# Kernel optimization log

Measured on AMD Instinct MI355X. Metric: run time of the kernel, lower is better.

## Reference

```python
import jax, jax.numpy as jnp
import numpy as np

N, S, D = 100000, 4, 256
TAU, ITERS = 0.1, 10
EPS = 1e-12  # torch F.normalize default eps


def sinkhorn_knopp(H_raw, tau=TAU, num_iters=ITERS):
    # H_raw: (N, S, S) -> doubly stochastic via exp + alternating row/col normalization
    M = jnp.exp(H_raw / tau)
    def body(_, M):
        M = M / jnp.sum(M, axis=-1, keepdims=True)  # row normalize
        M = M / jnp.sum(M, axis=-2, keepdims=True)  # col normalize
        return M
    return jax.lax.fori_loop(0, num_iters, body, M)


def setup_inputs() -> dict:
    key = jax.random.key(0)
    ks = jax.random.split(key, 7)
    x_streams = jax.random.normal(ks[0], (N, S, D), jnp.float32)
    message_output = jax.random.normal(ks[1], (N, D), jnp.float32)
    theta_pre = jax.random.normal(ks[2], (1, D), jnp.float32) * 0.01
    b_pre = jnp.ones((1, S), jnp.float32) / S
    theta_post = jax.random.normal(ks[3], (1, D), jnp.float32) * 0.01
    b_post = jnp.ones((1, S), jnp.float32) / S
    Theta_res = jax.random.normal(ks[4], (S, D), jnp.float32) * 0.01
    B_res = jnp.eye(S, dtype=jnp.float32) + jax.random.normal(ks[5], (S, S), jnp.float32) * 0.01
    alpha = jnp.asarray(0.01, jnp.float32)
    return {
        'x_streams': x_streams, 'message_output': message_output,
        'theta_pre': theta_pre, 'b_pre': b_pre,
        'theta_post': theta_post, 'b_post': b_post,
        'Theta_res': Theta_res, 'B_res': B_res,
        'alpha_pre': alpha, 'alpha_post': alpha, 'alpha_res': alpha,
    }


def reference(x_streams, message_output, theta_pre, b_pre, theta_post, b_post,
              Theta_res, B_res, alpha_pre, alpha_post, alpha_res):
    x = x_streams  # (N, S, D)
    # F.normalize(x, p=2, dim=-1)
    x_norm = x / jnp.maximum(jnp.linalg.norm(x, axis=-1, keepdims=True), EPS)
    x_pooled = x_norm.mean(axis=1)  # (N, D)

    # H_pre / H_post: (N, 1, S)
    dyn_pre = jnp.tanh(x_pooled @ theta_pre.T)   # (N, 1)
    H_pre = alpha_pre * dyn_pre[..., None] + b_pre[None, :, :]
    dyn_post = jnp.tanh(x_pooled @ theta_post.T)  # (N, 1)
    H_post = alpha_post * dyn_post[..., None] + b_post[None, :, :]

    # H_res: (N, S, S), doubly stochastic
    dyn_res = jnp.tanh(x_pooled @ Theta_res.T)   # (N, S)
    H_res_raw = alpha_res * dyn_res[..., None] + B_res[None, :, :]
    H_res = sinkhorn_knopp(H_res_raw, TAU, ITERS)

    residual = jnp.einsum('nst,ntd->nsd', H_res, x)          # bmm
    message_expanded = jnp.swapaxes(H_post, 1, 2) * message_output[:, None, :]  # (N,S,1)*(N,1,D)
    x_streams_new = residual + message_expanded
    return (x_streams_new, H_pre)
```

## Files before the change

### kernel.cpp

```cpp
#include <hip/hip_runtime.h>
#include <math.h>

static constexpr int DD = 256;

__device__ __forceinline__ float tanh_fast(float x) {
    float e = __expf(2.0f * x);
    return 1.0f - 2.0f * __builtin_amdgcn_rcpf(e + 1.0f);
}
__device__ __forceinline__ float dot4(float4 a, float4 b) {
    return a.x * b.x + a.y * b.y + a.z * b.z + a.w * b.w;
}
__device__ __forceinline__ float rl(float v, int l) {
    return __int_as_float(__builtin_amdgcn_readlane(__float_as_int(v), l));
}

__global__ __launch_bounds__(256) void hyperconn_kernel(
    const float* __restrict__ x_streams,
    const float* __restrict__ message_output,
    const float* __restrict__ theta_pre,
    const float* __restrict__ b_pre,
    const float* __restrict__ theta_post,
    const float* __restrict__ b_post,
    const float* __restrict__ Theta_res,
    const float* __restrict__ B_res,
    const float* __restrict__ alpha_pre_p,
    const float* __restrict__ alpha_post_p,
    const float* __restrict__ alpha_res_p,
    float* __restrict__ out_x,
    float* __restrict__ out_hpre,
    int Ntot)
{
    const int lane = threadIdx.x & 63;
    const int w = threadIdx.x >> 6;
    const long long n = (long long)blockIdx.x * 4 + w;
    const bool valid = (n < (long long)Ntot);

    __shared__ float sdots[4][8];
    __shared__ __align__(16) float sM[4][16];
    __shared__ __align__(16) float sHpost[4][4];

    float4 x0, x1, x2, x3, mv;
    if (valid) {
        const float4* xp = reinterpret_cast<const float4*>(x_streams + n * (4 * DD));
        x0 = xp[0 * 64 + lane];
        x1 = xp[1 * 64 + lane];
        x2 = xp[2 * 64 + lane];
        x3 = xp[3 * 64 + lane];
        mv = reinterpret_cast<const float4*>(message_output + n * DD)[lane];
    } else {
        x0 = x1 = x2 = x3 = mv = make_float4(0.f, 0.f, 0.f, 0.f);
    }
    const float4 tp = reinterpret_cast<const float4*>(theta_pre)[lane];
    const float4 tq = reinterpret_cast<const float4*>(theta_post)[lane];
    const float4 r0 = reinterpret_cast<const float4*>(Theta_res + 0 * DD)[lane];
    const float4 r1 = reinterpret_cast<const float4*>(Theta_res + 1 * DD)[lane];
    const float4 r2 = reinterpret_cast<const float4*>(Theta_res + 2 * DD)[lane];
    const float4 r3 = reinterpret_cast<const float4*>(Theta_res + 3 * DD)[lane];

    float ss0 = dot4(x0, x0), ss1 = dot4(x1, x1), ss2 = dot4(x2, x2), ss3 = dot4(x3, x3);

    const bool b0 = (lane & 1) != 0;
    const bool b1 = (lane & 2) != 0;
    const bool b2 = (lane & 4) != 0;
    {
        float sA = b0 ? ss0 : ss2, sB = b0 ? ss1 : ss3;
        float gA = __shfl_xor(sA, 1, 64), gB = __shfl_xor(sB, 1, 64);
        float A0 = (b0 ? ss2 : ss0) + gA;
        float A1 = (b0 ? ss3 : ss1) + gB;
        float s2 = b1 ? A0 : A1;
        float g2 = __shfl_xor(s2, 2, 64);
        float T = (b1 ? A1 : A0) + g2;
        T += __shfl_xor(T, 4, 64);
        T += __shfl_xor(T, 8, 64);
        T += __shfl_xor(T, 16, 64);
        T += __shfl_xor(T, 32, 64);
        ss0 = rl(T, 0); ss2 = rl(T, 1); ss1 = rl(T, 2); ss3 = rl(T, 3);
    }
    const float in0 = 0.25f * __builtin_amdgcn_rsqf(fmaxf(ss0, 1e-24f));
    const float in1 = 0.25f * __builtin_amdgcn_rsqf(fmaxf(ss1, 1e-24f));
    const float in2 = 0.25f * __builtin_amdgcn_rsqf(fmaxf(ss2, 1e-24f));
    const float in3 = 0.25f * __builtin_amdgcn_rsqf(fmaxf(ss3, 1e-24f));

    float4 p;
    p.x = in0 * x0.x + in1 * x1.x + in2 * x2.x + in3 * x3.x;
    p.y = in0 * x0.y + in1 * x1.y + in2 * x2.y + in3 * x3.y;
    p.z = in0 * x0.z + in1 * x1.z + in2 * x2.z + in3 * x3.z;
    p.w = in0 * x0.w + in1 * x1.w + in2 * x2.w + in3 * x3.w;

    float d0 = dot4(p, tp), d1 = dot4(p, tq);
    float d2 = dot4(p, r0), d3 = dot4(p, r1), d4 = dot4(p, r2), d5 = dot4(p, r3);

    {
        float sa = b0 ? d0 : d4, sb = b0 ? d1 : d5;
        float sc = b0 ? d2 : 0.0f, sd = b0 ? d3 : 0.0f;
        float ga = __shfl_xor(sa, 1, 64), gb = __shfl_xor(sb, 1, 64);
        float gc = __shfl_xor(sc, 1, 64), gd = __shfl_xor(sd, 1, 64);
        float B0 = (b0 ? d4 : d0) + ga;
        float B1 = (b0 ? d5 : d1) + gb;
        float B2 = (b0 ? 0.0f : d2) + gc;
        float B3 = (b0 ? 0.0f : d3) + gd;
        float s20 = b1 ? B0 : B2, s21 = b1 ? B1 : B3;
        float g20 = __shfl_xor(s20, 2, 64), g21 = __shfl_xor(s21, 2, 64);
        float C0 = (b1 ? B2 : B0) + g20;
        float C1 = (b1 ? B3 : B1) + g21;
        float s3 = b2 ? C0 : C1;
        float g3 = __shfl_xor(s3, 4, 64);
        float U = (b2 ? C1 : C0) + g3;
        U += __shfl_xor(U, 8, 64);
        U += __shfl_xor(U, 16, 64);
        U += __shfl_xor(U, 32, 64);
        int idx = ((lane & 1) << 2) | (lane & 2) | ((lane & 4) >> 2);
        if (lane < 8 && idx < 6) sdots[w][idx] = U;
    }
    __syncthreads();

    if (w == 0) {
        const int sw = lane >> 4, e = lane & 15, r = e >> 2;
        const float ares = alpha_res_p[0];
        float dres = tanh_fast(sdots[sw][2 + r]);
        float Mv = __expf((ares * dres + B_res[e]) * 10.0f);
#pragma unroll
        for (int it = 0; it < 10; ++it) {
            float a1 = Mv + __shfl_xor(Mv, 1, 64);
            float rs = a1 + __shfl_xor(a1, 2, 64);
            Mv *= __builtin_amdgcn_rcpf(rs);
            float c1 = Mv + __shfl_xor(Mv, 4, 64);
            float cs = c1 + __shfl_xor(c1, 8, 64);
            Mv *= __builtin_amdgcn_rcpf(cs);
        }
        sM[sw][e] = Mv;
    } else if (w == 1 && lane < 32) {
        const int sw = lane >> 3, h = (lane >> 2) & 1, c = lane & 3;
        float v = tanh_fast(sdots[sw][h]);
        if (h == 0) {
            long long nh = (long long)blockIdx.x * 4 + sw;
            if (nh < (long long)Ntot)
                out_hpre[nh * 4 + c] = alpha_pre_p[0] * v + b_pre[c];
        } else {
            sHpost[sw][c] = alpha_post_p[0] * v + b_post[c];
        }
    }
    __syncthreads();

    const float4 m0 = *reinterpret_cast<const float4*>(&sM[w][0]);
    const float4 m1 = *reinterpret_cast<const float4*>(&sM[w][4]);
    const float4 m2 = *reinterpret_cast<const float4*>(&sM[w][8]);
    const float4 m3 = *reinterpret_cast<const float4*>(&sM[w][12]);
    const float4 hp = *reinterpret_cast<const float4*>(&sHpost[w][0]);

    if (valid) {
        float4* op = reinterpret_cast<float4*>(out_x + n * (4 * DD));
        float4 o;
        o.x = m0.x * x0.x + m0.y * x1.x + m0.z * x2.x + m0.w * x3.x + hp.x * mv.x;
        o.y = m0.x * x0.y + m0.y * x1.y + m0.z * x2.y + m0.w * x3.y + hp.x * mv.y;
        o.z = m0.x * x0.z + m0.y * x1.z + m0.z * x2.z + m0.w * x3.z + hp.x * mv.z;
        o.w = m0.x * x0.w + m0.y * x1.w + m0.z * x2.w + m0.w * x3.w + hp.x * mv.w;
        op[0 * 64 + lane] = o;
        o.x = m1.x * x0.x + m1.y * x1.x + m1.z * x2.x + m1.w * x3.x + hp.y * mv.x;
        o.y = m1.x * x0.y + m1.y * x1.y + m1.z * x2.y + m1.w * x3.y + hp.y * mv.y;
        o.z = m1.x * x0.z + m1.y * x1.z + m1.z * x2.z + m1.w * x3.z + hp.y * mv.z;
        o.w = m1.x * x0.w + m1.y * x1.w + m1.z * x2.w + m1.w * x3.w + hp.y * mv.w;
        op[1 * 64 + lane] = o;
        o.x = m2.x * x0.x + m2.y * x1.x + m2.z * x2.x + m2.w * x3.x + hp.z * mv.x;
        o.y = m2.x * x0.y + m2.y * x1.y + m2.z * x2.y + m2.w * x3.y + hp.z * mv.y;
        o.z = m2.x * x0.z + m2.y * x1.z + m2.z * x2.z + m2.w * x3.z + hp.z * mv.z;
        o.w = m2.x * x0.w + m2.y * x1.w + m2.z * x2.w + m2.w * x3.w + hp.z * mv.w;
        op[2 * 64 + lane] = o;
        o.x = m3.x * x0.x + m3.y * x1.x + m3.z * x2.x + m3.w * x3.x + hp.w * mv.x;
        o.y = m3.x * x0.y + m3.y * x1.y + m3.z * x2.y + m3.w * x3.y + hp.w * mv.y;
        o.z = m3.x * x0.z + m3.y * x1.z + m3.z * x2.z + m3.w * x3.z + hp.w * mv.z;
        o.w = m3.x * x0.w + m3.y * x1.w + m3.z * x2.w + m3.w * x3.w + hp.w * mv.w;
        op[3 * 64 + lane] = o;
    }
}

extern "C" void kernel_launch(void* const* d_in, const int* in_sizes, int n_in,
                              void* d_out, int out_size, void* d_ws, size_t ws_size,
                              hipStream_t stream) {
    const float* x_streams      = (const float*)d_in[0];
    const float* message_output = (const float*)d_in[1];
    const float* theta_pre      = (const float*)d_in[2];
    const float* b_pre          = (const float*)d_in[3];
    const float* theta_post     = (const float*)d_in[4];
    const float* b_post         = (const float*)d_in[5];
    const float* Theta_res      = (const float*)d_in[6];
    const float* B_res          = (const float*)d_in[7];
    const float* alpha_pre      = (const float*)d_in[8];
    const float* alpha_post     = (const float*)d_in[9];
    const float* alpha_res      = (const float*)d_in[10];

    const int N = in_sizes[0] / (4 * DD);
    float* out_x = (float*)d_out;
    float* out_hpre = out_x + (size_t)N * 4 * DD;

    const int nblocks = (N + 3) / 4;
    hyperconn_kernel<<<nblocks, 256, 0, stream>>>(
        x_streams, message_output, theta_pre, b_pre, theta_post, b_post,
        Theta_res, B_res, alpha_pre, alpha_post, alpha_res, out_x, out_hpre, N);
}
```

Baseline: 165.0 us.

## Persistent grid-stride waves with register prefetch, DPP reductions, no shared memory

The kernel becomes persistent: a fixed grid of 2048 blocks where each wavefront loops over rows in grid-stride order and prefetches the next row's x and message into registers while computing the current one. Cross-lane reductions and the Sinkhorn iterations now use DPP quad/row ops plus readlane instead of ds_swizzle shuffles. Each wave computes its own Sinkhorn and H_post, removing the shared-memory staging and both __syncthreads. The intent is to hide memory latency and cut sync and LDS overhead. The cost is higher register pressure from the prefetch buffers and redundant per-wave Sinkhorn work.

```diff
diff --git a/kernel.cpp b/kernel.cpp
--- a/kernel.cpp
+++ b/kernel.cpp
@@ -3,6 +3,16 @@
 
 static constexpr int DD = 256;
 
+static constexpr int QXOR1 = 0xB1;
+static constexpr int QXOR2 = 0x4E;
+static constexpr int ROR4  = 0x124;
+static constexpr int ROR8  = 0x128;
+
+template <int CTRL>
+__device__ __forceinline__ float dpp_add(float v) {
+    int p = __builtin_amdgcn_update_dpp(0, __float_as_int(v), CTRL, 0xF, 0xF, true);
+    return v + __int_as_float(p);
+}
 __device__ __forceinline__ float tanh_fast(float x) {
     float e = __expf(2.0f * x);
     return 1.0f - 2.0f * __builtin_amdgcn_rcpf(e + 1.0f);
@@ -31,146 +41,154 @@
     int Ntot)
 {
     const int lane = threadIdx.x & 63;
-    const int w = threadIdx.x >> 6;
-    const long long n = (long long)blockIdx.x * 4 + w;
-    const bool valid = (n < (long long)Ntot);
-
-    __shared__ float sdots[4][8];
-    __shared__ __align__(16) float sM[4][16];
-    __shared__ __align__(16) float sHpost[4][4];
-
-    float4 x0, x1, x2, x3, mv;
-    if (valid) {
-        const float4* xp = reinterpret_cast<const float4*>(x_streams + n * (4 * DD));
-        x0 = xp[0 * 64 + lane];
-        x1 = xp[1 * 64 + lane];
-        x2 = xp[2 * 64 + lane];
-        x3 = xp[3 * 64 + lane];
-        mv = reinterpret_cast<const float4*>(message_output + n * DD)[lane];
-    } else {
-        x0 = x1 = x2 = x3 = mv = make_float4(0.f, 0.f, 0.f, 0.f);
-    }
+    const int gw = blockIdx.x * (blockDim.x >> 6) + (threadIdx.x >> 6);
+    const int W = gridDim.x * (blockDim.x >> 6);
+
     const float4 tp = reinterpret_cast<const float4*>(theta_pre)[lane];
     const float4 tq = reinterpret_cast<const float4*>(theta_post)[lane];
     const float4 r0 = reinterpret_cast<const float4*>(Theta_res + 0 * DD)[lane];
     const float4 r1 = reinterpret_cast<const float4*>(Theta_res + 1 * DD)[lane];
     const float4 r2 = reinterpret_cast<const float4*>(Theta_res + 2 * DD)[lane];
     const float4 r3 = reinterpret_cast<const float4*>(Theta_res + 3 * DD)[lane];
-
-    float ss0 = dot4(x0, x0), ss1 = dot4(x1, x1), ss2 = dot4(x2, x2), ss3 = dot4(x3, x3);
-
-    const bool b0 = (lane & 1) != 0;
-    const bool b1 = (lane & 2) != 0;
-    const bool b2 = (lane & 4) != 0;
-    {
-        float sA = b0 ? ss0 : ss2, sB = b0 ? ss1 : ss3;
-        float gA = __shfl_xor(sA, 1, 64), gB = __shfl_xor(sB, 1, 64);
-        float A0 = (b0 ? ss2 : ss0) + gA;
-        float A1 = (b0 ? ss3 : ss1) + gB;
-        float s2 = b1 ? A0 : A1;
-        float g2 = __shfl_xor(s2, 2, 64);
-        float T = (b1 ? A1 : A0) + g2;
-        T += __shfl_xor(T, 4, 64);
-        T += __shfl_xor(T, 8, 64);
-        T += __shfl_xor(T, 16, 64);
-        T += __shfl_xor(T, 32, 64);
-        ss0 = rl(T, 0); ss2 = rl(T, 1); ss1 = rl(T, 2); ss3 = rl(T, 3);
+    const float Bres_l = B_res[lane & 15];
+    const float bpre_l = b_pre[lane & 3];
+    const float apre = alpha_pre_p[0], apost = alpha_post_p[0], ares = alpha_res_p[0];
+    const float bp0 = b_post[0], bp1 = b_post[1], bp2 = b_post[2], bp3 = b_post[3];
+
+    const bool hi32 = (lane & 32) != 0;
+    const bool hi16 = (lane & 16) != 0;
+    const int r_id = (lane >> 2) & 3;
+
+    long long n = gw;
+    float4 cx0, cx1, cx2, cx3, cmv;
+    if (n < (long long)Ntot) {
+        const float4* xp = reinterpret_cast<const float4*>(x_streams + n * (4LL * DD));
+        cx0 = xp[0 * 64 + lane];
+        cx1 = xp[1 * 64 + lane];
+        cx2 = xp[2 * 64 + lane];
+        cx3 = xp[3 * 64 + lane];
+        cmv = reinterpret_cast<const float4*>(message_output + n * DD)[lane];
     }
-    const float in0 = 0.25f * __builtin_amdgcn_rsqf(fmaxf(ss0, 1e-24f));
-    const float in1 = 0.25f * __builtin_amdgcn_rsqf(fmaxf(ss1, 1e-24f));
-    const float in2 = 0.25f * __builtin_amdgcn_rsqf(fmaxf(ss2, 1e-24f));
-    const float in3 = 0.25f * __builtin_amdgcn_rsqf(fmaxf(ss3, 1e-24f));
-
-    float4 p;
-    p.x = in0 * x0.x + in1 * x1.x + in2 * x2.x + in3 * x3.x;
-    p.y = in0 * x0.y + in1 * x1.y + in2 * x2.y + in3 * x3.y;
-    p.z = in0 * x0.z + in1 * x1.z + in2 * x2.z + in3 * x3.z;
-    p.w = in0 * x0.w + in1 * x1.w + in2 * x2.w + in3 * x3.w;
-
-    float d0 = dot4(p, tp), d1 = dot4(p, tq);
-    float d2 = dot4(p, r0), d3 = dot4(p, r1), d4 = dot4(p, r2), d5 = dot4(p, r3);
-
-    {
-        float sa = b0 ? d0 : d4, sb = b0 ? d1 : d5;
-        float sc = b0 ? d2 : 0.0f, sd = b0 ? d3 : 0.0f;
-        float ga = __shfl_xor(sa, 1, 64), gb = __shfl_xor(sb, 1, 64);
-        float gc = __shfl_xor(sc, 1, 64), gd = __shfl_xor(sd, 1, 64);
-        float B0 = (b0 ? d4 : d0) + ga;
-        float B1 = (b0 ? d5 : d1) + gb;
-        float B2 = (b0 ? 0.0f : d2) + gc;
-        float B3 = (b0 ? 0.0f : d3) + gd;
-        float s20 = b1 ? B0 : B2, s21 = b1 ? B1 : B3;
-        float g20 = __shfl_xor(s20, 2, 64), g21 = __shfl_xor(s21, 2, 64);
-        float C0 = (b1 ? B2 : B0) + g20;
-        float C1 = (b1 ? B3 : B1) + g21;
-        float s3 = b2 ? C0 : C1;
-        float g3 = __shfl_xor(s3, 4, 64);
-        float U = (b2 ? C1 : C0) + g3;
-        U += __shfl_xor(U, 8, 64);
-        U += __shfl_xor(U, 16, 64);
-        U += __shfl_xor(U, 32, 64);
-        int idx = ((lane & 1) << 2) | (lane & 2) | ((lane & 4) >> 2);
-        if (lane < 8 && idx < 6) sdots[w][idx] = U;
-    }
-    __syncthreads();
-
-    if (w == 0) {
-        const int sw = lane >> 4, e = lane & 15, r = e >> 2;
-        const float ares = alpha_res_p[0];
-        float dres = tanh_fast(sdots[sw][2 + r]);
-        float Mv = __expf((ares * dres + B_res[e]) * 10.0f);
+
+    while (n < (long long)Ntot) {
+        const long long nn = n + W;
+        float4 px0, px1, px2, px3, pmv;
+        if (nn < (long long)Ntot) {
+            const float4* xp = reinterpret_cast<const float4*>(x_streams + nn * (4LL * DD));
+            px0 = xp[0 * 64 + lane];
+            px1 = xp[1 * 64 + lane];
+            px2 = xp[2 * 64 + lane];
+            px3 = xp[3 * 64 + lane];
+            pmv = reinterpret_cast<const float4*>(message_output + nn * DD)[lane];
+        }
+
+        float ss0 = dot4(cx0, cx0), ss1 = dot4(cx1, cx1);
+        float ss2 = dot4(cx2, cx2), ss3 = dot4(cx3, cx3);
+
+        {
+            float sA = hi32 ? ss0 : ss2;
+            float sB = hi32 ? ss1 : ss3;
+            float gA = __shfl_xor(sA, 32, 64);
+            float gB = __shfl_xor(sB, 32, 64);
+            float A0 = (hi32 ? ss2 : ss0) + gA;
+            float A1 = (hi32 ? ss3 : ss1) + gB;
+            float s2 = hi16 ? A0 : A1;
+            float g2 = __shfl_xor(s2, 16, 64);
+            float B = (hi16 ? A1 : A0) + g2;
+            B = dpp_add<QXOR1>(B);
+            B = dpp_add<QXOR2>(B);
+            B = dpp_add<ROR4>(B);
+            B = dpp_add<ROR8>(B);
+            ss0 = rl(B, 0); ss1 = rl(B, 16); ss2 = rl(B, 32); ss3 = rl(B, 48);
+        }
+        const float in0 = 0.25f * __builtin_amdgcn_rsqf(fmaxf(ss0, 1e-24f));
+        const float in1 = 0.25f * __builtin_amdgcn_rsqf(fmaxf(ss1, 1e-24f));
+        const float in2 = 0.25f * __builtin_amdgcn_rsqf(fmaxf(ss2, 1e-24f));
+        const float in3 = 0.25f * __builtin_amdgcn_rsqf(fmaxf(ss3, 1e-24f));
+
+        float4 p;
+        p.x = in0 * cx0.x + in1 * cx1.x + in2 * cx2.x + in3 * cx3.x;
+        p.y = in0 * cx0.y + in1 * cx1.y + in2 * cx2.y + in3 * cx3.y;
+        p.z = in0 * cx0.z + in1 * cx1.z + in2 * cx2.z + in3 * cx3.z;
+        p.w = in0 * cx0.w + in1 * cx1.w + in2 * cx2.w + in3 * cx3.w;
+
+        float d0 = dot4(p, tp), d1 = dot4(p, tq);
+        float d2 = dot4(p, r0), d3 = dot4(p, r1), d4 = dot4(p, r2), d5 = dot4(p, r3);
+
+        {
+            float sA = hi32 ? d0 : d3;
+            float sB = hi32 ? d1 : d4;
+            float sC = hi32 ? d2 : d5;
+            float gA = __shfl_xor(sA, 32, 64);
+            float gB = __shfl_xor(sB, 32, 64);
+            float gC = __shfl_xor(sC, 32, 64);
+            float A0 = (hi32 ? d3 : d0) + gA;
+            float A1 = (hi32 ? d4 : d1) + gB;
+            float A2 = (hi32 ? d5 : d2) + gC;
+            float e1s = hi16 ? A0 : A2;
+            float e1g = __shfl_xor(e1s, 16, 64);
+            float e2g = __shfl_xor(A1, 16, 64);
+            float R0 = hi16 ? (A2 + e1g) : (A0 + e1g);
+            float R1 = A1 + e2g;
+            R0 = dpp_add<QXOR1>(R0); R1 = dpp_add<QXOR1>(R1);
+            R0 = dpp_add<QXOR2>(R0); R1 = dpp_add<QXOR2>(R1);
+            R0 = dpp_add<ROR4>(R0);  R1 = dpp_add<ROR4>(R1);
+            R0 = dpp_add<ROR8>(R0);  R1 = dpp_add<ROR8>(R1);
+            d0 = rl(R0, 0);  d1 = rl(R1, 0);
+            d2 = rl(R0, 16);
+            d3 = rl(R0, 32); d4 = rl(R1, 32);
+            d5 = rl(R0, 48);
+        }
+
+        const float td0 = tanh_fast(d0);
+        const float td1 = tanh_fast(d1);
+        const float td2 = tanh_fast(d2), td3 = tanh_fast(d3);
+        const float td4 = tanh_fast(d4), td5 = tanh_fast(d5);
+
+        float dsel = (r_id < 2) ? (r_id == 0 ? td2 : td3) : (r_id == 2 ? td4 : td5);
+        float Mv = __expf(fmaf(ares, dsel, Bres_l) * 10.0f);
 #pragma unroll
         for (int it = 0; it < 10; ++it) {
-            float a1 = Mv + __shfl_xor(Mv, 1, 64);
-            float rs = a1 + __shfl_xor(a1, 2, 64);
+            float rs = dpp_add<QXOR2>(dpp_add<QXOR1>(Mv));
             Mv *= __builtin_amdgcn_rcpf(rs);
-            float c1 = Mv + __shfl_xor(Mv, 4, 64);
-            float cs = c1 + __shfl_xor(c1, 8, 64);
+            float cs = dpp_add<ROR8>(dpp_add<ROR4>(Mv));
             Mv *= __builtin_amdgcn_rcpf(cs);
         }
-        sM[sw][e] = Mv;
-    } else if (w == 1 && lane < 32) {
-        const int sw = lane >> 3, h = (lane >> 2) & 1, c = lane & 3;
-        float v = tanh_fast(sdots[sw][h]);
-        if (h == 0) {
-            long long nh = (long long)blockIdx.x * 4 + sw;
-            if (nh < (long long)Ntot)
-                out_hpre[nh * 4 + c] = alpha_pre_p[0] * v + b_pre[c];
-        } else {
-            sHpost[sw][c] = alpha_post_p[0] * v + b_post[c];
-        }
-    }
-    __syncthreads();
-
-    const float4 m0 = *reinterpret_cast<const float4*>(&sM[w][0]);
-    const float4 m1 = *reinterpret_cast<const float4*>(&sM[w][4]);
-    const float4 m2 = *reinterpret_cast<const float4*>(&sM[w][8]);
-    const float4 m3 = *reinterpret_cast<const float4*>(&sM[w][12]);
-    const float4 hp = *reinterpret_cast<const float4*>(&sHpost[w][0]);
-
-    if (valid) {
-        float4* op = reinterpret_cast<float4*>(out_x + n * (4 * DD));
+
+        const float m00 = rl(Mv, 0),  m01 = rl(Mv, 1),  m02 = rl(Mv, 2),  m03 = rl(Mv, 3);
+        const float m10 = rl(Mv, 4),  m11 = rl(Mv, 5),  m12 = rl(Mv, 6),  m13 = rl(Mv, 7);
+        const float m20 = rl(Mv, 8),  m21 = rl(Mv, 9),  m22 = rl(Mv, 10), m23 = rl(Mv, 11);
+        const float m30 = rl(Mv, 12), m31 = rl(Mv, 13), m32 = rl(Mv, 14), m33 = rl(Mv, 15);
+        const float hp0 = fmaf(apost, td1, bp0), hp1 = fmaf(apost, td1, bp1);
+        const float hp2 = fmaf(apost, td1, bp2), hp3 = fmaf(apost, td1, bp3);
+
+        if (lane < 4) out_hpre[n * 4 + lane] = fmaf(apre, td0, bpre_l);
+
+        float4* op = reinterpret_cast<float4*>(out_x + n * (4LL * DD));
         float4 o;
-        o.x = m0.x * x0.x + m0.y * x1.x + m0.z * x2.x + m0.w * x3.x + hp.x * mv.x;
-        o.y = m0.x * x0.y + m0.y * x1.y + m0.z * x2.y + m0.w * x3.y + hp.x * mv.y;
-        o.z = m0.x * x0.z + m0.y * x1.z + m0.z * x2.z + m0.w * x3.z + hp.x * mv.z;
-        o.w = m0.x * x0.w + m0.y * x1.w + m0.z * x2.w + m0.w * x3.w + hp.x * mv.w;
+        o.x = m00 * cx0.x + m01 * cx1.x + m02 * cx2.x + m03 * cx3.x + hp0 * cmv.x;
+        o.y = m00 * cx0.y + m01 * cx1.y + m02 * cx2.y + m03 * cx3.y + hp0 * cmv.y;
+        o.z = m00 * cx0.z + m01 * cx1.z + m02 * cx2.z + m03 * cx3.z + hp0 * cmv.z;
+        o.w = m00 * cx0.w + m01 * cx1.w + m02 * cx2.w + m03 * cx3.w + hp0 * cmv.w;
         op[0 * 64 + lane] = o;
-        o.x = m1.x * x0.x + m1.y * x1.x + m1.z * x2.x + m1.w * x3.x + hp.y * mv.x;
-        o.y = m1.x * x0.y + m1.y * x1.y + m1.z * x2.y + m1.w * x3.y + hp.y * mv.y;
-        o.z = m1.x * x0.z + m1.y * x1.z + m1.z * x2.z + m1.w * x3.z + hp.y * mv.z;
-        o.w = m1.x * x0.w + m1.y * x1.w + m1.z * x2.w + m1.w * x3.w + hp.y * mv.w;
+        o.x = m10 * cx0.x + m11 * cx1.x + m12 * cx2.x + m13 * cx3.x + hp1 * cmv.x;
+        o.y = m10 * cx0.y + m11 * cx1.y + m12 * cx2.y + m13 * cx3.y + hp1 * cmv.y;
+        o.z = m10 * cx0.z + m11 * cx1.z + m12 * cx2.z + m13 * cx3.z + hp1 * cmv.z;
+        o.w = m10 * cx0.w + m11 * cx1.w + m12 * cx2.w + m13 * cx3.w + hp1 * cmv.w;
         op[1 * 64 + lane] = o;
-        o.x = m2.x * x0.x + m2.y * x1.x + m2.z * x2.x + m2.w * x3.x + hp.z * mv.x;
-        o.y = m2.x * x0.y + m2.y * x1.y + m2.z * x2.y + m2.w * x3.y + hp.z * mv.y;
-        o.z = m2.x * x0.z + m2.y * x1.z + m2.z * x2.z + m2.w * x3.z + hp.z * mv.z;
-        o.w = m2.x * x0.w + m2.y * x1.w + m2.z * x2.w + m2.w * x3.w + hp.z * mv.w;
+        o.x = m20 * cx0.x + m21 * cx1.x + m22 * cx2.x + m23 * cx3.x + hp2 * cmv.x;
+        o.y = m20 * cx0.y + m21 * cx1.y + m22 * cx2.y + m23 * cx3.y + hp2 * cmv.y;
+        o.z = m20 * cx0.z + m21 * cx1.z + m22 * cx2.z + m23 * cx3.z + hp2 * cmv.z;
+        o.w = m20 * cx0.w + m21 * cx1.w + m22 * cx2.w + m23 * cx3.w + hp2 * cmv.w;
         op[2 * 64 + lane] = o;
-        o.x = m3.x * x0.x + m3.y * x1.x + m3.z * x2.x + m3.w * x3.x + hp.w * mv.x;
-        o.y = m3.x * x0.y + m3.y * x1.y + m3.z * x2.y + m3.w * x3.y + hp.w * mv.y;
-        o.z = m3.x * x0.z + m3.y * x1.z + m3.z * x2.z + m3.w * x3.z + hp.w * mv.z;
-        o.w = m3.x * x0.w + m3.y * x1.w + m3.z * x2.w + m3.w * x3.w + hp.w * mv.w;
+        o.x = m30 * cx0.x + m31 * cx1.x + m32 * cx2.x + m33 * cx3.x + hp3 * cmv.x;
+        o.y = m30 * cx0.y + m31 * cx1.y + m32 * cx2.y + m33 * cx3.y + hp3 * cmv.y;
+        o.z = m30 * cx0.z + m31 * cx1.z + m32 * cx2.z + m33 * cx3.z + hp3 * cmv.z;
+        o.w = m30 * cx0.w + m31 * cx1.w + m32 * cx2.w + m33 * cx3.w + hp3 * cmv.w;
         op[3 * 64 + lane] = o;
+
+        cx0 = px0; cx1 = px1; cx2 = px2; cx3 = px3; cmv = pmv;
+        n = nn;
     }
 }
 
@@ -193,7 +211,7 @@
     float* out_x = (float*)d_out;
     float* out_hpre = out_x + (size_t)N * 4 * DD;
 
-    const int nblocks = (N + 3) / 4;
+    const int nblocks = 2048;
     hyperconn_kernel<<<nblocks, 256, 0, stream>>>(
         x_streams, message_output, theta_pre, b_pre, theta_post, b_post,
         Theta_res, B_res, alpha_pre, alpha_post, alpha_res, out_x, out_hpre, N);
```

Measured after the change: 181.5 us. 1.1x slower.
